# Performance work log

Hardware: AMD Instinct MI355X
Metric: run time of the kernel (lower is better)

Reference implementation:

```python
import jax, jax.numpy as jnp
import numpy as np
from jax.scipy.special import logsumexp

EPS = 1e-12  # torch F.normalize eps
SINKHORN_ITERS = 3


def _l2norm(a, axis):
    n = jnp.sqrt(jnp.sum(a * a, axis=axis, keepdims=True))
    return a / jnp.maximum(n, EPS)


def _log_optimal_transport(scores, alpha, iters):
    # scores: [B, m, n]; alpha: scalar dust-bin param
    b, m, n = scores.shape
    bins = jnp.broadcast_to(alpha, (b, 1, n)).astype(scores.dtype)
    Z = jnp.concatenate([scores, bins], axis=1)  # [B, m+1, n]
    norm = -np.log(float(m + n))
    log_mu = jnp.asarray(
        np.concatenate([np.full(m, norm), [np.log(float(n - m)) + norm]]),
        scores.dtype,
    )  # [m+1]
    log_nu = jnp.full((n,), norm, scores.dtype)
    u = jnp.zeros((b, m + 1), scores.dtype)
    v = jnp.zeros((b, n), scores.dtype)
    for _ in range(iters):
        u = log_mu[None, :] - logsumexp(Z + v[:, None, :], axis=2)
        v = log_nu[None, :] - logsumexp(Z + u[:, :, None], axis=1)
    return Z + u[:, :, None] + v[:, None, :] - norm


def _forward(x, t, tw1, tb1, tw2, tb2, cw1, cb1, cw2, cb2, sw1, sb1, sw2, sb2, dust_bin):
    B, C = x.shape[0], x.shape[1]
    xf = x.reshape(B, C, -1)  # [B, C, N], 1x1 convs act per-location
    # cluster features f: [B, l, N]
    h = jax.nn.relu(jnp.einsum('oc,bcn->bon', cw1, xf) + cb1[None, :, None])
    f = jnp.einsum('oc,bcn->bon', cw2, h) + cb2[None, :, None]
    # global token: [B, g]
    tok = jax.nn.relu(t @ tw1.T + tb1) @ tw2.T + tb2
    # assignment scores p: [B, m, N]
    hs = jax.nn.relu(jnp.einsum('oc,bcn->bon', sw1, xf) + sb1[None, :, None])
    p = jnp.einsum('oc,bcn->bon', sw2, hs) + sb2[None, :, None]
    Z = _log_optimal_transport(p, dust_bin, SINKHORN_ITERS)
    P = jnp.exp(Z)[:, :-1, :]  # drop dust bin row -> [B, m, N]
    # VLAD-style aggregation: the repeat/multiply/sum is just a batched matmul
    agg = jnp.einsum('bln,bmn->blm', f, P)  # [B, l, m]
    agg = _l2norm(agg, axis=1).reshape(B, -1)  # intra-normalize over l, flatten l-major
    out = jnp.concatenate([_l2norm(tok, axis=-1), agg], axis=-1)
    return _l2norm(out, axis=-1)


def setup_inputs() -> dict:
    key = jax.random.key(0)
    ks = jax.random.split(key, 14)
    B, C, H, W = 64, 768, 32, 32
    L, M, G, HID = 128, 64, 256, 512

    def p(k, shape):
        return jax.random.normal(k, shape, jnp.float32) * 0.02

    return {
        'x': jax.random.normal(ks[0], (B, C, H, W), jnp.float32),
        't': jax.random.normal(ks[1], (B, C), jnp.float32),
        'tw1': p(ks[2], (HID, C)), 'tb1': jnp.zeros((HID,), jnp.float32),
        'tw2': p(ks[3], (G, HID)), 'tb2': jnp.zeros((G,), jnp.float32),
        'cw1': p(ks[4], (HID, C)), 'cb1': jnp.zeros((HID,), jnp.float32),
        'cw2': p(ks[5], (L, HID)), 'cb2': jnp.zeros((L,), jnp.float32),
        'sw1': p(ks[6], (HID, C)), 'sb1': jnp.zeros((HID,), jnp.float32),
        'sw2': p(ks[7], (M, HID)), 'sb2': jnp.zeros((M,), jnp.float32),
        'dust_bin': jnp.asarray(1.0, jnp.float32),
    }


def reference(x, t, tw1, tb1, tw2, tb2, cw1, cb1, cw2, cb2, sw1, sb1, sw2, sb2, dust_bin):
    return _forward(x, t, tw1, tb1, tw2, tb2, cw1, cb1, cw2, cb2, sw1, sb1, sw2, sb2, dust_bin)
```

## Files before the change

### kernel.cpp

```cpp
#include <hip/hip_runtime.h>
#include <math.h>


#define B_SZ   64
#define C_IN   768
#define N_LOC  1024
#define HID    512
#define L_DIM  128
#define M_DIM  64
#define G_DIM  256
#define OUTD   (G_DIM + L_DIM * M_DIM)

typedef unsigned short u16;
typedef __bf16 bf16x8 __attribute__((ext_vector_type(8)));
typedef float f32x4 __attribute__((ext_vector_type(4)));

typedef const __attribute__((address_space(1))) void* gptr_t;
typedef __attribute__((address_space(3))) void* sptr_t;

__device__ __forceinline__ void load_lds16(const void* g, void* l) {
    __builtin_amdgcn_global_load_lds((gptr_t)g, (sptr_t)l, 16, 0, 0);
}

__device__ __forceinline__ u16 f2bf(float f) {
    unsigned u = __float_as_uint(f);
    u += 0x7fffu + ((u >> 16) & 1u);
    return (u16)(u >> 16);
}
__device__ __forceinline__ float bf2f(u16 h) {
    return __uint_as_float(((unsigned)h) << 16);
}

__device__ __forceinline__ float waveReduceSum(float v) {
#pragma unroll
    for (int off = 32; off > 0; off >>= 1) v += __shfl_xor(v, off, 64);
    return v;
}

__global__ __launch_bounds__(256) void setup_kernel(
        const float* __restrict__ cw1, const float* __restrict__ sw1,
        const float* __restrict__ cw2, const float* __restrict__ sw2,
        u16* __restrict__ cw1p, u16* __restrict__ sw1p,
        u16* __restrict__ cw2p, u16* __restrict__ sw2p,
        const float* __restrict__ t, const float* __restrict__ tw1,
        const float* __restrict__ tb1, float* __restrict__ hidb) {
    __shared__ __align__(16) float tl[C_IN];
    const int blk = blockIdx.x;
    const int tid = threadIdx.x;

    if (blk < 432) {
        const int q = blk * 256 + tid;
        const float* src;
        u16* dst;
        if (q < 98304) {
            int path = q / 49152, r = q % 49152;
            int kch = r / 512, c = r & 511;
            src = (path ? sw1 : cw1) + (size_t)c * C_IN + kch * 8;
            dst = (path ? sw1p : cw1p) + (size_t)r * 8;
        } else {
            int q2 = q - 98304;
            int path = (q2 >= 8192) ? 1 : 0;
            int r = q2 - (path ? 8192 : 0);
            int S2 = path ? M_DIM : L_DIM;
            int k2 = r / (4 * S2), kc = (r / S2) & 3, c = r % S2;
            src = (path ? sw2 : cw2) + (size_t)c * HID + k2 * 32 + kc * 8;
            dst = (path ? sw2p : cw2p) + (size_t)r * 8;
        }
        float4 v0 = *(const float4*)(src);
        float4 v1 = *(const float4*)(src + 4);
        *(ushort4*)(dst) = make_ushort4(f2bf(v0.x), f2bf(v0.y), f2bf(v0.z), f2bf(v0.w));
        *(ushort4*)(dst + 4) = make_ushort4(f2bf(v1.x), f2bf(v1.y), f2bf(v1.z), f2bf(v1.w));
        return;
    }

    const int by = blk - 432;
    const int j0 = (by & 7) * 64;
    const int b = by >> 3;
    const int lane = tid & 63;
    const int wave = tid >> 6;
    for (int i = tid; i < C_IN; i += 256) tl[i] = t[(size_t)b * C_IN + i];
    __syncthreads();
    for (int j = wave; j < 64; j += 4) {
        const int row = j0 + j;
        const float4* wr = (const float4*)(tw1 + (size_t)row * C_IN);
        const float4* tr = (const float4*)tl;
        float s = 0.f;
#pragma unroll
        for (int q = 0; q < 3; ++q) {
            float4 wv = wr[lane + 64 * q];
            float4 tv = tr[lane + 64 * q];
            s += wv.x * tv.x + wv.y * tv.y + wv.z * tv.z + wv.w * tv.w;
        }
        s = waveReduceSum(s);
        if (lane == 0) hidb[(size_t)b * HID + row] = fmaxf(s + tb1[row], 0.f);
    }
}

__global__ __launch_bounds__(256) void transpose_x(const float* __restrict__ x,
                                                   u16* __restrict__ xP) {
    __shared__ float tile[64][65];
    const int n0 = blockIdx.x * 64;
    const int c0 = blockIdx.y * 64;
    const size_t b = blockIdx.z;
    const float* xb = x + b * (size_t)(C_IN * N_LOC);
    u16* xpb = xP + b * (size_t)(N_LOC * C_IN);
    const int tid = threadIdx.x;

    const int jn = (tid & 15) * 4;
    const int cr = tid >> 4;
#pragma unroll
    for (int r = 0; r < 4; ++r) {
        int c = cr + r * 16;
        float4 v = *(const float4*)(xb + (size_t)(c0 + c) * N_LOC + n0 + jn);
        tile[c][jn + 0] = v.x;
        tile[c][jn + 1] = v.y;
        tile[c][jn + 2] = v.z;
        tile[c][jn + 3] = v.w;
    }
    __syncthreads();

    const int n = tid & 63;
    const int ch0 = tid >> 6;
    const int nG = n0 + n;
#pragma unroll
    for (int r = 0; r < 2; ++r) {
        const int ch = ch0 + r * 4;
        const int cG = c0 + ch * 8;
        u16* dst = xpb + (size_t)(nG >> 6) * (64 * C_IN) + (cG >> 5) * 2048 +
                   ((cG & 31) >> 3) * 512 + (nG & 63) * 8;
        ushort4 o0 = make_ushort4(f2bf(tile[ch * 8 + 0][n]), f2bf(tile[ch * 8 + 1][n]),
                                  f2bf(tile[ch * 8 + 2][n]), f2bf(tile[ch * 8 + 3][n]));
        ushort4 o1 = make_ushort4(f2bf(tile[ch * 8 + 4][n]), f2bf(tile[ch * 8 + 5][n]),
                                  f2bf(tile[ch * 8 + 6][n]), f2bf(tile[ch * 8 + 7][n]));
        *(ushort4*)(dst) = o0;
        *(ushort4*)(dst + 4) = o1;
    }
}

__global__ __launch_bounds__(256, 2) void fused12(
        const u16* __restrict__ xP,
        const u16* __restrict__ cw1p, const float* __restrict__ cb1,
        const u16* __restrict__ cw2p, const float* __restrict__ cb2,
        const u16* __restrict__ sw1p, const float* __restrict__ sb1,
        const u16* __restrict__ sw2p, const float* __restrict__ sb2,
        u16* __restrict__ fT, u16* __restrict__ pT) {
    __shared__ __align__(16) u16 LDSu[36864];
    const int tid = threadIdx.x;
    const int lane = tid & 63;
    const int wc = tid >> 6;

    const int id = blockIdx.x + 16 * blockIdx.y + 32 * blockIdx.z;
    const int nid = (id & 7) * 256 + (id >> 3);
    const int bx = nid & 15;
    const int path = (nid >> 4) & 1;
    const int bz = nid >> 5;
    const int r0 = bx * 64;

    const u16* W1p = path ? sw1p : cw1p;
    const float* B1 = path ? sb1 : cb1;
    const u16* W2p = path ? sw2p : cw2p;
    const float* B2 = path ? sb2 : cb2;
    u16* O2 = path ? pT : fT;
    const int S2 = path ? M_DIM : L_DIM;

    const u16* Ap = xP + (size_t)bz * N_LOC * C_IN + (size_t)bx * (64 * C_IN);

    f32x4 acc1[4][8];
#pragma unroll
    for (int mi = 0; mi < 4; ++mi)
#pragma unroll
        for (int ni = 0; ni < 8; ++ni)
            acc1[mi][ni] = (f32x4){0.f, 0.f, 0.f, 0.f};

    const int nk = C_IN / 32;

#define STG_A(db_, kt_)                                                        \
    load_lds16(Ap + (size_t)(kt_) * 2048 + tid * 8, &LDSu[(db_) * 2048 + tid * 8])
#define STG_B(db_, kt_)                                                        \
    do {                                                                       \
        _Pragma("unroll")                                                      \
        for (int j_ = 0; j_ < 8; ++j_)                                         \
            load_lds16(W1p + (size_t)(kt_) * 16384 + (size_t)(j_ * 256 + tid) * 8, \
                       &LDSu[4096 + (db_) * 16384 + (j_ * 256 + tid) * 8]);    \
    } while (0)

#define AV_PTR(db_, mi_)                                                       \
    ((const bf16x8*)&LDSu[(db_) * 2048 + (lane >> 4) * 512 +                   \
                          (16 * (mi_) + (lane & 15)) * 8])
#define BW_PTR(db_, ni_)                                                       \
    ((const bf16x8*)&LDSu[4096 + (db_) * 16384 + (lane >> 4) * 4096 +          \
                          (128 * wc + 16 * (ni_) + (lane & 15)) * 8])

    STG_A(0, 0);
    STG_B(0, 0);
    STG_A(1, 1);
    asm volatile("s_waitcnt vmcnt(1)" ::: "memory");
    __builtin_amdgcn_s_barrier();

    for (int t = 0; t < nk; ++t) {
        const int db = t & 1;
        bf16x8 av[4], bw[8];

#pragma unroll
        for (int mi = 0; mi < 4; ++mi) av[mi] = *AV_PTR(db, mi);
#pragma unroll
        for (int ni = 0; ni < 8; ++ni) bw[ni] = *BW_PTR(db, ni);
        if (t + 1 < nk) STG_B(db ^ 1, t + 1);

        asm volatile("s_waitcnt lgkmcnt(0)" ::: "memory");
        __builtin_amdgcn_sched_barrier(0);
        __builtin_amdgcn_s_barrier();

        if (t + 2 < nk) STG_A(db, t + 2);

        __builtin_amdgcn_s_setprio(1);
#pragma unroll
        for (int mi = 0; mi < 4; ++mi)
#pragma unroll
            for (int ni = 0; ni < 8; ++ni)
                acc1[mi][ni] = __builtin_amdgcn_mfma_f32_16x16x32_bf16(
                    av[mi], bw[ni], acc1[mi][ni], 0, 0, 0);
        __builtin_amdgcn_s_setprio(0);
        __builtin_amdgcn_sched_barrier(0);

        if (t + 2 < nk)
            asm volatile("s_waitcnt vmcnt(1)" ::: "memory");
        else
            asm volatile("s_waitcnt vmcnt(0)" ::: "memory");
        __builtin_amdgcn_s_barrier();
    }
#undef STG_A
#undef STG_B
#undef AV_PTR
#undef BW_PTR

    {
        float bv1[8];
#pragma unroll
        for (int ni = 0; ni < 8; ++ni)
            bv1[ni] = B1[128 * wc + 16 * ni + (lane & 15)];
#pragma unroll
        for (int mi = 0; mi < 4; ++mi)
#pragma unroll
            for (int ni = 0; ni < 8; ++ni)
#pragma unroll
                for (int rr = 0; rr < 4; ++rr) {
                    int n = 16 * mi + (lane >> 4) * 4 + rr;
                    int c = 128 * wc + 16 * ni + (lane & 15);
                    float v = fmaxf(acc1[mi][ni][rr] + bv1[ni], 0.f);
                    LDSu[(c >> 3) * 512 + n * 8 + (c & 7)] = f2bf(v);
                }
    }
    __syncthreads();

    f32x4 acc2[4][2];
#pragma unroll
    for (int mi = 0; mi < 4; ++mi) {
        acc2[mi][0] = (f32x4){0.f, 0.f, 0.f, 0.f};
        acc2[mi][1] = (f32x4){0.f, 0.f, 0.f, 0.f};
    }
    const int c2base = (S2 == L_DIM) ? 32 * wc : 16 * wc;
    const int cA = c2base + (lane & 15);
    const int cB = c2base + 16 + (lane & 15);
    const int fb0 = (lane >> 4) * S2 + cA;
    const int fb1 = (lane >> 4) * S2 + cB;

    bf16x8 w0n = *(const bf16x8*)(W2p + (size_t)fb0 * 8);
    bf16x8 w1n = {};
    if (S2 == L_DIM) w1n = *(const bf16x8*)(W2p + (size_t)fb1 * 8);

    for (int k2 = 0; k2 < 16; ++k2) {
        bf16x8 w0 = w0n, w1 = w1n;
        if (k2 < 15) {
            w0n = *(const bf16x8*)(W2p + ((size_t)(k2 + 1) * 4 * S2 + fb0) * 8);
            if (S2 == L_DIM)
                w1n = *(const bf16x8*)(W2p + ((size_t)(k2 + 1) * 4 * S2 + fb1) * 8);
        }
        bf16x8 a2[4];
#pragma unroll
        for (int mi = 0; mi < 4; ++mi)
            a2[mi] = *(const bf16x8*)&LDSu[(k2 * 4 + (lane >> 4)) * 512 +
                                           (16 * mi + (lane & 15)) * 8];
#pragma unroll
        for (int mi = 0; mi < 4; ++mi) {
            acc2[mi][0] = __builtin_amdgcn_mfma_f32_16x16x32_bf16(
                a2[mi], w0, acc2[mi][0], 0, 0, 0);
            if (S2 == L_DIM)
                acc2[mi][1] = __builtin_amdgcn_mfma_f32_16x16x32_bf16(
                    a2[mi], w1, acc2[mi][1], 0, 0, 0);
        }
    }

    const float b20 = B2[cA];
    const float b21 = (S2 == L_DIM) ? B2[cB] : 0.f;
    u16* Ob = O2 + (size_t)bz * N_LOC * S2;
#pragma unroll
    for (int mi = 0; mi < 4; ++mi)
#pragma unroll
        for (int rr = 0; rr < 4; ++rr) {
            int row = r0 + 16 * mi + (lane >> 4) * 4 + rr;
            Ob[(size_t)row * S2 + cA] = f2bf(acc2[mi][0][rr] + b20);
            if (S2 == L_DIM)
                Ob[(size_t)row * S2 + cB] = f2bf(acc2[mi][1][rr] + b21);
        }
}

__global__ __launch_bounds__(1024) void sinkhorn_kernel(const u16* __restrict__ pT,
                                                        const float* __restrict__ dust,
                                                        u16* __restrict__ PTb) {
    __shared__ u16 sp[M_DIM][N_LOC];
    __shared__ float eu[M_DIM + 1];
    __shared__ float ev[N_LOC];
    const int b = blockIdx.x;
    const int t = threadIdx.x;
    const int lane = t & 63;
    const int wave = t >> 6;
    const float alpha = dust[0];
    const float Ea = __expf(alpha);
    const float mu = 1.f / 1088.f;
    const float mu64 = 960.f / 1088.f;
    const float nu = 1.f / 1088.f;

    const uint4* prow = (const uint4*)(pT + ((size_t)b * N_LOC + t) * M_DIM);
#pragma unroll
    for (int q = 0; q < 8; ++q) {
        uint4 ch = prow[q];
        sp[q * 8 + 0][t] = (u16)(ch.x);
        sp[q * 8 + 1][t] = (u16)(ch.x >> 16);
        sp[q * 8 + 2][t] = (u16)(ch.y);
        sp[q * 8 + 3][t] = (u16)(ch.y >> 16);
        sp[q * 8 + 4][t] = (u16)(ch.z);
        sp[q * 8 + 5][t] = (u16)(ch.z >> 16);
        sp[q * 8 + 6][t] = (u16)(ch.w);
        sp[q * 8 + 7][t] = (u16)(ch.w >> 16);
    }
#pragma unroll
    for (int m = 0; m < M_DIM; ++m)
        sp[m][t] = f2bf(__expf(bf2f(sp[m][t])));
    ev[t] = 1.f;
    __syncthreads();

    for (int it = 0; it < 3; ++it) {
        for (int m = wave; m < M_DIM + 1; m += 16) {
            float s = 0.f;
            if (m < M_DIM) {
#pragma unroll
                for (int q = 0; q < 16; ++q) {
                    int c = lane + 64 * q;
                    s += bf2f(sp[m][c]) * ev[c];
                }
            } else {
#pragma unroll
                for (int q = 0; q < 16; ++q) {
                    int c = lane + 64 * q;
                    s += ev[c];
                }
                s *= Ea;
            }
            s = waveReduceSum(s);
            if (lane == 0) eu[m] = ((m < M_DIM) ? mu : mu64) / s;
        }
        __syncthreads();
        float s = Ea * eu[M_DIM];
#pragma unroll 8
        for (int m = 0; m < M_DIM; ++m) s += bf2f(sp[m][t]) * eu[m];
        ev[t] = nu / s;
        __syncthreads();
    }

    const float evt = ev[t] * 1088.f;
    u16* Prow = PTb + ((size_t)b * N_LOC + t) * M_DIM;
#pragma unroll
    for (int m8 = 0; m8 < M_DIM; m8 += 8) {
        unsigned v0 = f2bf(bf2f(sp[m8 + 0][t]) * eu[m8 + 0] * evt);
        unsigned v1 = f2bf(bf2f(sp[m8 + 1][t]) * eu[m8 + 1] * evt);
        unsigned v2 = f2bf(bf2f(sp[m8 + 2][t]) * eu[m8 + 2] * evt);
        unsigned v3 = f2bf(bf2f(sp[m8 + 3][t]) * eu[m8 + 3] * evt);
        unsigned v4 = f2bf(bf2f(sp[m8 + 4][t]) * eu[m8 + 4] * evt);
        unsigned v5 = f2bf(bf2f(sp[m8 + 5][t]) * eu[m8 + 5] * evt);
        unsigned v6 = f2bf(bf2f(sp[m8 + 6][t]) * eu[m8 + 6] * evt);
        unsigned v7 = f2bf(bf2f(sp[m8 + 7][t]) * eu[m8 + 7] * evt);
        uint4 w;
        w.x = v0 | (v1 << 16);
        w.y = v2 | (v3 << 16);
        w.z = v4 | (v5 << 16);
        w.w = v6 | (v7 << 16);
        *(uint4*)(Prow + m8) = w;
    }
}

__global__ __launch_bounds__(256) void agg_final_kernel(
        const u16* __restrict__ fT, const u16* __restrict__ PTb,
        const float* __restrict__ hidb, const float* __restrict__ tw2,
        const float* __restrict__ tb2, float* __restrict__ out) {
    __shared__ __align__(16) float SH[9760];
    const int b = blockIdx.y;
    const int bx = blockIdx.x;
    const int tid = threadIdx.x;
    const int lane = tid & 63;
    const int wave = tid >> 6;
    const float EPS = 1e-12f;
    const float rs65 = 1.f / sqrtf(65.f);
    float* ob = out + (size_t)b * OUTD;

    if (bx == 4) {
        float* hl = SH;
        float* tk = SH + 512;
        float* red = SH + 768;
        for (int i = tid; i < HID; i += 256) hl[i] = hidb[(size_t)b * HID + i];
        __syncthreads();
        for (int j = wave; j < G_DIM; j += 4) {
            const float4* wr = (const float4*)(tw2 + (size_t)j * HID);
            const float4* hr = (const float4*)hl;
            float s = 0.f;
#pragma unroll
            for (int q = 0; q < 2; ++q) {
                float4 wv = wr[lane + 64 * q];
                float4 hv = hr[lane + 64 * q];
                s += wv.x * hv.x + wv.y * hv.y + wv.z * hv.z + wv.w * hv.w;
            }
            s = waveReduceSum(s);
            if (lane == 0) tk[j] = s + tb2[j];
        }
        __syncthreads();
        const float tv = tk[tid];
        float ssl = tv * tv;
        ssl = waveReduceSum(ssl);
        if (lane == 0) red[wave] = ssl;
        __syncthreads();
        const float stok = red[0] + red[1] + red[2] + red[3];
        const float rt = rs65 / fmaxf(sqrtf(stok), EPS);
        ob[tid] = tv * rt;
        return;
    }

    const int m0 = bx * 16;
    float* Fs = SH;
    float* Ps = SH + 8448;
    float* ag = SH;
    float* rm = SH + 9728;
    const u16* fb = fT + (size_t)b * N_LOC * L_DIM;
    const u16* Pb = PTb + (size_t)b * N_LOC * M_DIM;

    const int sn = tid >> 2;
    const int fl = (tid & 3) * 32;
    const int pm = (tid & 3) * 4;
    const int tl = (tid >> 3) * 4;
    const int tm = (tid & 7) * 2;

    float acc[4][2] = {};

    for (int n0 = 0; n0 < N_LOC; n0 += 64) {
        __syncthreads();
#pragma unroll
        for (int j = 0; j < 4; ++j) {
            uint4 ld = *(const uint4*)(fb + (size_t)(n0 + sn) * L_DIM + fl + j * 8);
            float4 lo = make_float4(bf2f((u16)(ld.x)), bf2f((u16)(ld.x >> 16)),
                                    bf2f((u16)(ld.y)), bf2f((u16)(ld.y >> 16)));
            float4 hi = make_float4(bf2f((u16)(ld.z)), bf2f((u16)(ld.z >> 16)),
                                    bf2f((u16)(ld.w)), bf2f((u16)(ld.w >> 16)));
            *(float4*)&Fs[sn * 132 + fl + j * 8] = lo;
            *(float4*)&Fs[sn * 132 + fl + j * 8 + 4] = hi;
        }
        {
            uint2 ld = *(const uint2*)(Pb + (size_t)(n0 + sn) * M_DIM + m0 + pm);
            float4 v = make_float4(bf2f((u16)(ld.x)), bf2f((u16)(ld.x >> 16)),
                                   bf2f((u16)(ld.y)), bf2f((u16)(ld.y >> 16)));
            *(float4*)&Ps[sn * 20 + pm] = v;
        }
        __syncthreads();
#pragma unroll 8
        for (int nn = 0; nn < 64; ++nn) {
            float4 a = *(const float4*)&Fs[nn * 132 + tl];
            float p0 = Ps[nn * 20 + tm];
            float p1 = Ps[nn * 20 + tm + 1];
            acc[0][0] = fmaf(a.x, p0, acc[0][0]);
            acc[0][1] = fmaf(a.x, p1, acc[0][1]);
            acc[1][0] = fmaf(a.y, p0, acc[1][0]);
            acc[1][1] = fmaf(a.y, p1, acc[1][1]);
            acc[2][0] = fmaf(a.z, p0, acc[2][0]);
            acc[2][1] = fmaf(a.z, p1, acc[2][1]);
            acc[3][0] = fmaf(a.w, p0, acc[3][0]);
            acc[3][1] = fmaf(a.w, p1, acc[3][1]);
        }
    }

    __syncthreads();
#pragma unroll
    for (int i = 0; i < 4; ++i) {
        ag[(tl + i) * 17 + tm] = acc[i][0];
        ag[(tl + i) * 17 + tm + 1] = acc[i][1];
    }
    __syncthreads();
    if (tid < 16) {
        float ss = 0.f;
#pragma unroll 8
        for (int l = 0; l < L_DIM; ++l) {
            float xv = ag[l * 17 + tid];
            ss = fmaf(xv, xv, ss);
        }
        rm[tid] = rs65 / fmaxf(sqrtf(ss), EPS);
    }
    __syncthreads();
    const float r0 = rm[tm];
    const float r1 = rm[tm + 1];
#pragma unroll
    for (int i = 0; i < 4; ++i) {
        ob[G_DIM + (tl + i) * M_DIM + m0 + tm] = acc[i][0] * r0;
        ob[G_DIM + (tl + i) * M_DIM + m0 + tm + 1] = acc[i][1] * r1;
    }
}

extern "C" void kernel_launch(void* const* d_in, const int* in_sizes, int n_in,
                              void* d_out, int out_size, void* d_ws, size_t ws_size,
                              hipStream_t stream) {
    const float* x    = (const float*)d_in[0];
    const float* t    = (const float*)d_in[1];
    const float* tw1  = (const float*)d_in[2];
    const float* tb1  = (const float*)d_in[3];
    const float* tw2  = (const float*)d_in[4];
    const float* tb2  = (const float*)d_in[5];
    const float* cw1  = (const float*)d_in[6];
    const float* cb1  = (const float*)d_in[7];
    const float* cw2  = (const float*)d_in[8];
    const float* cb2  = (const float*)d_in[9];
    const float* sw1  = (const float*)d_in[10];
    const float* sb1  = (const float*)d_in[11];
    const float* sw2  = (const float*)d_in[12];
    const float* sb2  = (const float*)d_in[13];
    const float* dust = (const float*)d_in[14];
    float* out = (float*)d_out;

    char* ws = (char*)d_ws;
    u16* xP    = (u16*)(ws);
    u16* fT    = (u16*)(ws + 100663296ull);
    u16* pT    = (u16*)(ws + 117440512ull);
    u16* cw1p  = (u16*)(ws + 125829120ull);
    u16* sw1p  = (u16*)(ws + 126615552ull);
    u16* cw2p  = (u16*)(ws + 127401984ull);
    u16* sw2p  = (u16*)(ws + 127533056ull);
    float* hidb = (float*)(ws + 127598592ull);
    u16* PTb   = (u16*)(ws);

    setup_kernel<<<944, 256, 0, stream>>>(cw1, sw1, cw2, sw2,
                                          cw1p, sw1p, cw2p, sw2p,
                                          t, tw1, tb1, hidb);
    transpose_x<<<dim3(N_LOC / 64, C_IN / 64, B_SZ), 256, 0, stream>>>(x, xP);

    fused12<<<dim3(16, 2, B_SZ), 256, 0, stream>>>(
        xP, cw1p, cb1, cw2p, cb2, sw1p, sb1, sw2p, sb2, fT, pT);

    sinkhorn_kernel<<<B_SZ, 1024, 0, stream>>>(pT, dust, PTb);
    agg_final_kernel<<<dim3(5, B_SZ), 256, 0, stream>>>(fT, PTb, hidb, tw2, tb2, out);
}
```

Before: 273.6 us.

## Fuse x transpose and bf16 conversion into the first GEMM's A-tile staging

Removes the separate transpose_x kernel, which wrote a bf16 blocked copy of x to workspace. fused12 now reads fp32 x directly with per-thread scalar loads strided by N_LOC, converts to bf16 in registers, and writes packed tiles into LDS, using register double-buffering across an unrolled pair of k-steps. This saves one kernel launch and a full write and re-read of the transposed activations. In exchange, each x element is read in fp32 by both path blocks, and the A-operand loads become scalar register loads rather than async global-to-LDS copies, which may raise register pressure and memory latency inside the GEMM loop.

```diff
diff --git a/kernel.cpp b/kernel.cpp
--- a/kernel.cpp
+++ b/kernel.cpp
@@ -96,49 +96,8 @@
     }
 }
 
-__global__ __launch_bounds__(256) void transpose_x(const float* __restrict__ x,
-                                                   u16* __restrict__ xP) {
-    __shared__ float tile[64][65];
-    const int n0 = blockIdx.x * 64;
-    const int c0 = blockIdx.y * 64;
-    const size_t b = blockIdx.z;
-    const float* xb = x + b * (size_t)(C_IN * N_LOC);
-    u16* xpb = xP + b * (size_t)(N_LOC * C_IN);
-    const int tid = threadIdx.x;
-
-    const int jn = (tid & 15) * 4;
-    const int cr = tid >> 4;
-#pragma unroll
-    for (int r = 0; r < 4; ++r) {
-        int c = cr + r * 16;
-        float4 v = *(const float4*)(xb + (size_t)(c0 + c) * N_LOC + n0 + jn);
-        tile[c][jn + 0] = v.x;
-        tile[c][jn + 1] = v.y;
-        tile[c][jn + 2] = v.z;
-        tile[c][jn + 3] = v.w;
-    }
-    __syncthreads();
-
-    const int n = tid & 63;
-    const int ch0 = tid >> 6;
-    const int nG = n0 + n;
-#pragma unroll
-    for (int r = 0; r < 2; ++r) {
-        const int ch = ch0 + r * 4;
-        const int cG = c0 + ch * 8;
-        u16* dst = xpb + (size_t)(nG >> 6) * (64 * C_IN) + (cG >> 5) * 2048 +
-                   ((cG & 31) >> 3) * 512 + (nG & 63) * 8;
-        ushort4 o0 = make_ushort4(f2bf(tile[ch * 8 + 0][n]), f2bf(tile[ch * 8 + 1][n]),
-                                  f2bf(tile[ch * 8 + 2][n]), f2bf(tile[ch * 8 + 3][n]));
-        ushort4 o1 = make_ushort4(f2bf(tile[ch * 8 + 4][n]), f2bf(tile[ch * 8 + 5][n]),
-                                  f2bf(tile[ch * 8 + 6][n]), f2bf(tile[ch * 8 + 7][n]));
-        *(ushort4*)(dst) = o0;
-        *(ushort4*)(dst + 4) = o1;
-    }
-}
-
 __global__ __launch_bounds__(256, 2) void fused12(
-        const u16* __restrict__ xP,
+        const float* __restrict__ x,
         const u16* __restrict__ cw1p, const float* __restrict__ cb1,
         const u16* __restrict__ cw2p, const float* __restrict__ cb2,
         const u16* __restrict__ sw1p, const float* __restrict__ sb1,
@@ -163,7 +122,8 @@
     u16* O2 = path ? pT : fT;
     const int S2 = path ? M_DIM : L_DIM;
 
-    const u16* Ap = xP + (size_t)bz * N_LOC * C_IN + (size_t)bx * (64 * C_IN);
+    const float* xb = x + (size_t)bz * C_IN * N_LOC + r0 + (tid & 63) +
+                      (size_t)(tid >> 6) * 8 * N_LOC;
 
     f32x4 acc1[4][8];
 #pragma unroll
@@ -174,8 +134,23 @@
 
     const int nk = C_IN / 32;
 
-#define STG_A(db_, kt_)                                                        \
-    load_lds16(Ap + (size_t)(kt_) * 2048 + tid * 8, &LDSu[(db_) * 2048 + tid * 8])
+#define XLOAD(XR_, kt_)                                                        \
+    do {                                                                       \
+        _Pragma("unroll")                                                      \
+        for (int j_ = 0; j_ < 8; ++j_)                                         \
+            XR_[j_] = xb[(size_t)((kt_) * 32 + j_) * N_LOC];                   \
+    } while (0)
+
+#define AWRITE(db_, XR_)                                                       \
+    do {                                                                       \
+        uint4 w_;                                                              \
+        w_.x = (unsigned)f2bf(XR_[0]) | ((unsigned)f2bf(XR_[1]) << 16);        \
+        w_.y = (unsigned)f2bf(XR_[2]) | ((unsigned)f2bf(XR_[3]) << 16);        \
+        w_.z = (unsigned)f2bf(XR_[4]) | ((unsigned)f2bf(XR_[5]) << 16);        \
+        w_.w = (unsigned)f2bf(XR_[6]) | ((unsigned)f2bf(XR_[7]) << 16);        \
+        *(uint4*)(&LDSu[(db_) * 2048 + tid * 8]) = w_;                         \
+    } while (0)
+
 #define STG_B(db_, kt_)                                                        \
     do {                                                                       \
         _Pragma("unroll")                                                      \
@@ -191,48 +166,55 @@
     ((const bf16x8*)&LDSu[4096 + (db_) * 16384 + (lane >> 4) * 4096 +          \
                           (128 * wc + 16 * (ni_) + (lane & 15)) * 8])
 
-    STG_A(0, 0);
+#define TILE_BODY(T_, DB_, XC_, XN_)                                           \
+    {                                                                          \
+        bf16x8 av[4], bw[8];                                                   \
+        _Pragma("unroll")                                                      \
+        for (int mi = 0; mi < 4; ++mi) av[mi] = *AV_PTR(DB_, mi);              \
+        _Pragma("unroll")                                                      \
+        for (int ni = 0; ni < 8; ++ni) bw[ni] = *BW_PTR(DB_, ni);              \
+        if ((T_) + 1 < nk) STG_B((DB_) ^ 1, (T_) + 1);                         \
+        if ((T_) + 2 < nk) XLOAD(XN_, (T_) + 2);                               \
+        asm volatile("s_waitcnt lgkmcnt(0)" ::: "memory");                     \
+        __builtin_amdgcn_sched_barrier(0);                                     \
+        __builtin_amdgcn_s_barrier();                                          \
+        if ((T_) + 1 < nk) AWRITE((DB_) ^ 1, XC_);                             \
+        __builtin_amdgcn_s_setprio(1);                                         \
+        _Pragma("unroll")                                                      \
+        for (int mi = 0; mi < 4; ++mi)                                         \
+            _Pragma("unroll")                                                  \
+            for (int ni = 0; ni < 8; ++ni)                                     \
+                acc1[mi][ni] = __builtin_amdgcn_mfma_f32_16x16x32_bf16(        \
+                    av[mi], bw[ni], acc1[mi][ni], 0, 0, 0);                    \
+        __builtin_amdgcn_s_setprio(0);                                         \
+        __builtin_amdgcn_sched_barrier(0);                                     \
+        asm volatile("s_waitcnt lgkmcnt(0)" ::: "memory");                     \
+        if ((T_) + 2 < nk)                                                     \
+            asm volatile("s_waitcnt vmcnt(8)" ::: "memory");                   \
+        else                                                                   \
+            asm volatile("s_waitcnt vmcnt(0)" ::: "memory");                   \
+        __builtin_amdgcn_s_barrier();                                          \
+    }
+
+    float xrA[8], xrB[8];
+
     STG_B(0, 0);
-    STG_A(1, 1);
-    asm volatile("s_waitcnt vmcnt(1)" ::: "memory");
+    XLOAD(xrA, 0);
+    AWRITE(0, xrA);
+    XLOAD(xrB, 1);
+    asm volatile("s_waitcnt lgkmcnt(0)" ::: "memory");
     __builtin_amdgcn_s_barrier();
 
-    for (int t = 0; t < nk; ++t) {
-        const int db = t & 1;
-        bf16x8 av[4], bw[8];
-
-#pragma unroll
-        for (int mi = 0; mi < 4; ++mi) av[mi] = *AV_PTR(db, mi);
-#pragma unroll
-        for (int ni = 0; ni < 8; ++ni) bw[ni] = *BW_PTR(db, ni);
-        if (t + 1 < nk) STG_B(db ^ 1, t + 1);
-
-        asm volatile("s_waitcnt lgkmcnt(0)" ::: "memory");
-        __builtin_amdgcn_sched_barrier(0);
-        __builtin_amdgcn_s_barrier();
-
-        if (t + 2 < nk) STG_A(db, t + 2);
-
-        __builtin_amdgcn_s_setprio(1);
-#pragma unroll
-        for (int mi = 0; mi < 4; ++mi)
-#pragma unroll
-            for (int ni = 0; ni < 8; ++ni)
-                acc1[mi][ni] = __builtin_amdgcn_mfma_f32_16x16x32_bf16(
-                    av[mi], bw[ni], acc1[mi][ni], 0, 0, 0);
-        __builtin_amdgcn_s_setprio(0);
-        __builtin_amdgcn_sched_barrier(0);
-
-        if (t + 2 < nk)
-            asm volatile("s_waitcnt vmcnt(1)" ::: "memory");
-        else
-            asm volatile("s_waitcnt vmcnt(0)" ::: "memory");
-        __builtin_amdgcn_s_barrier();
-    }
-#undef STG_A
+    for (int tt = 0; tt < nk; tt += 2) {
+        TILE_BODY(tt, 0, xrB, xrA);
+        TILE_BODY(tt + 1, 1, xrA, xrB);
+    }
+#undef XLOAD
+#undef AWRITE
 #undef STG_B
 #undef AV_PTR
 #undef BW_PTR
+#undef TILE_BODY
 
     {
         float bv1[8];
@@ -532,7 +514,6 @@
     float* out = (float*)d_out;
 
     char* ws = (char*)d_ws;
-    u16* xP    = (u16*)(ws);
     u16* fT    = (u16*)(ws + 100663296ull);
     u16* pT    = (u16*)(ws + 117440512ull);
     u16* cw1p  = (u16*)(ws + 125829120ull);
@@ -545,10 +526,9 @@
     setup_kernel<<<944, 256, 0, stream>>>(cw1, sw1, cw2, sw2,
                                           cw1p, sw1p, cw2p, sw2p,
                                           t, tw1, tb1, hidb);
-    transpose_x<<<dim3(N_LOC / 64, C_IN / 64, B_SZ), 256, 0, stream>>>(x, xP);
 
     fused12<<<dim3(16, 2, B_SZ), 256, 0, stream>>>(
-        xP, cw1p, cb1, cw2p, cb2, sw1p, sb1, sw2p, sb2, fT, pT);
+        x, cw1p, cb1, cw2p, cb2, sw1p, sb1, sw2p, sb2, fT, pT);
 
     sinkhorn_kernel<<<B_SZ, 1024, 0, stream>>>(pT, dust, PTb);
     agg_final_kernel<<<dim3(5, B_SZ), 256, 0, stream>>>(fT, PTb, hidb, tw2, tb2, out);
```

Measured after the change: 253.4 us. 1.08x faster.
